# Kernel optimization log

Hardware: AMD Instinct MI355X
Metric: run time of the kernel (lower is better)

The kernel has to match this reference:

```python
import jax, jax.numpy as jnp
import numpy as np

N, E, H, IN, B, L, OUT = 50000, 600000, 128, 128, 256, 4, 10
BN_EPS = 1e-5


def setup_inputs() -> dict:
    key = jax.random.key(0)
    ks = jax.random.split(key, 12)
    x = jax.random.normal(ks[0], (N, IN), dtype=jnp.float32)
    edge_index = jax.random.randint(ks[1], (2, E), 0, N, dtype=jnp.int64)
    batch = jnp.sort(jax.random.randint(ks[2], (N,), 0, B, dtype=jnp.int64))
    s_in = 1.0 / np.sqrt(IN)
    s_h = 1.0 / np.sqrt(H)
    W_enc = jax.random.uniform(ks[3], (IN, H), jnp.float32, -s_in, s_in)
    b_enc = jax.random.uniform(ks[4], (H,), jnp.float32, -s_in, s_in)
    W = jax.random.uniform(ks[5], (L, H, H), jnp.float32, -s_h, s_h)
    b = jax.random.uniform(ks[6], (L, H), jnp.float32, -s_h, s_h)
    gamma = jnp.ones((L, H), jnp.float32)
    beta = jnp.zeros((L, H), jnp.float32)
    W_cls = jax.random.uniform(ks[7], (H, OUT), jnp.float32, -s_h, s_h)
    b_cls = jax.random.uniform(ks[8], (OUT,), jnp.float32, -s_h, s_h)
    return {"x": x, "edge_index": edge_index, "batch": batch,
            "W_enc": W_enc, "b_enc": b_enc, "W": W, "b": b,
            "gamma": gamma, "beta": beta, "W_cls": W_cls, "b_cls": b_cls}


def reference(x, edge_index, batch, W_enc, b_enc, W, b, gamma, beta, W_cls, b_cls):
    n = x.shape[0]
    # add self-loops (PyG GCNConv default)
    loop = jnp.arange(n, dtype=edge_index.dtype)
    row = jnp.concatenate([edge_index[0], loop])  # source nodes
    col = jnp.concatenate([edge_index[1], loop])  # target nodes
    # symmetric normalization: deg over targets, norm_e = d^-1/2[src] * d^-1/2[dst]
    deg = jax.ops.segment_sum(jnp.ones_like(col, dtype=x.dtype), col, num_segments=n)
    dinv = jnp.where(deg > 0, jax.lax.rsqrt(deg), 0.0)
    norm = dinv[row] * dinv[col]  # [E+N]

    # encoder (plain Linear since use_atom_encoder=False)
    h = x @ W_enc + b_enc

    for l in range(L):
        # GCNConv: transform, normalized scatter-add, bias
        t = h @ W[l]
        msg = norm[:, None] * t[row]               # [E+N, H] gather
        agg = jax.ops.segment_sum(msg, col, num_segments=n) + b[l]
        # BatchNorm1d (batch statistics, training-mode math)
        mean = jnp.mean(agg, axis=0)
        var = jnp.var(agg, axis=0)
        hn = (agg - mean) * jax.lax.rsqrt(var + BN_EPS) * gamma[l] + beta[l]
        h = jax.nn.relu(hn)  # dropout p=0.0 -> identity

    # global mean pool over graphs
    sums = jax.ops.segment_sum(h, batch, num_segments=B)
    counts = jax.ops.segment_sum(jnp.ones((n,), h.dtype), batch, num_segments=B)
    g = sums / jnp.maximum(counts, 1.0)[:, None]
    return g @ W_cls + b_cls
```

## Files before the change

### kernel.cpp

```cpp
#include <hip/hip_runtime.h>

#define NN 50000
#define NE 600000
#define HD 128
#define NL 4
#define NB 256
#define NO 10
#define BN_EPS 1e-5f

typedef short bf16x8 __attribute__((ext_vector_type(8)));
typedef float f32x4 __attribute__((ext_vector_type(4)));

__device__ __forceinline__ unsigned short f2bf(float f) {
    union { float f; unsigned int u; } x; x.f = f;
    unsigned int u = x.u;
    unsigned int r = (u + 0x7FFFu + ((u >> 16) & 1u)) >> 16;
    return (unsigned short)r;
}
__device__ __forceinline__ float bf2f(unsigned short s) {
    union { unsigned int u; float f; } x; x.u = ((unsigned int)s) << 16;
    return x.f;
}


__global__ void hist_kernel(const int* __restrict__ col, int* __restrict__ cnt, int e) {
    int i = blockIdx.x * blockDim.x + threadIdx.x;
    if (i < e) atomicAdd(&cnt[col[i]], 1);
}

__global__ void scan1_kernel(const int* __restrict__ cnt, int* __restrict__ outp,
                             int* __restrict__ bsums, float* __restrict__ dinv,
                             int M, int n) {
    __shared__ int s[256];
    int tid = threadIdx.x;
    int base = blockIdx.x * 1024 + tid * 4;
    int v[4];
#pragma unroll
    for (int j = 0; j < 4; ++j) {
        int idx = base + j;
        v[j] = (idx < n) ? cnt[idx] : 0;
        if (idx < n) dinv[idx] = rsqrtf((float)(v[j] + 1));
    }
    int tot = v[0] + v[1] + v[2] + v[3];
    s[tid] = tot;
    __syncthreads();
    for (int off = 1; off < 256; off <<= 1) {
        int x = (tid >= off) ? s[tid - off] : 0;
        __syncthreads();
        s[tid] += x;
        __syncthreads();
    }
    int run = (tid == 0) ? 0 : s[tid - 1];
#pragma unroll
    for (int j = 0; j < 4; ++j) {
        int idx = base + j;
        if (idx < M) outp[idx] = run;
        run += v[j];
    }
    if (tid == 255) bsums[blockIdx.x] = s[255];
}

__global__ void scan3_kernel(int* __restrict__ outp, const int* __restrict__ bsums, int M) {
    __shared__ int sb[64];
    int tid = threadIdx.x;
    int seg = blockIdx.x >> 2;
    if (tid < 64) sb[tid] = (tid < seg) ? bsums[tid] : 0;
    __syncthreads();
    if (tid < 32) sb[tid] += sb[tid + 32];
    __syncthreads();
    if (tid < 16) sb[tid] += sb[tid + 16];
    __syncthreads();
    if (tid < 8) sb[tid] += sb[tid + 8];
    __syncthreads();
    if (tid < 4) sb[tid] += sb[tid + 4];
    __syncthreads();
    if (tid < 2) sb[tid] += sb[tid + 2];
    __syncthreads();
    if (tid == 0) sb[0] += sb[1];
    __syncthreads();
    int i = blockIdx.x * 256 + tid;
    if (i < M) outp[i] += sb[0];
}

__global__ void place_kernel(const int* __restrict__ row, const int* __restrict__ col,
                             const float* __restrict__ dinv, const int* __restrict__ rp,
                             int* __restrict__ fill, int2* __restrict__ csr, int e) {
    int i = blockIdx.x * blockDim.x + threadIdx.x;
    if (i < e) {
        int r = row[i], c = col[i];
        int pos = atomicAdd(&fill[c], 1);
        int idx = rp[c] + pos;
        csr[idx] = make_int2(r, __float_as_int(dinv[r] * dinv[c]));
    }
}

__global__ void wconv_kernel(const float* __restrict__ W, unsigned short* __restrict__ Wt) {
    int i = blockIdx.x * blockDim.x + threadIdx.x;
    if (i >= 4 * 16384) return;
    int m = i >> 14;
    int r = (i >> 7) & 127;
    int k = i & 127;
    Wt[16384 + i] = f2bf(W[(size_t)m * 16384 + k * 128 + r]);
}

__global__ void fuse_enc_kernel(const float* __restrict__ W_enc, const float* __restrict__ W0,
                                const float* __restrict__ b_enc,
                                unsigned short* __restrict__ WtK, float* __restrict__ bb) {
    if (blockIdx.x < 64) {
        int gid = blockIdx.x * 256 + threadIdx.x;
        int i = gid & 127, o = gid >> 7;
        float s = 0.f;
#pragma unroll 8
        for (int h = 0; h < 128; ++h) s += W_enc[i * 128 + h] * W0[h * 128 + o];
        WtK[o * 128 + i] = f2bf(s);
    } else if (threadIdx.x < 128) {
        int o = threadIdx.x;
        float s = 0.f;
#pragma unroll 8
        for (int h = 0; h < 128; ++h) s += b_enc[h] * W0[h * 128 + o];
        bb[o] = s;
    }
}

template <int AMODE>
__global__ __launch_bounds__(256) void gemm128_mfma(const void* __restrict__ Ap,
                                                    const unsigned short* __restrict__ Wt,
                                                    const float* __restrict__ bias,
                                                    const float* __restrict__ bnp,
                                                    unsigned short* __restrict__ Cp,
                                                    int nrows) {
    int wave = threadIdx.x >> 6;
    int lane = threadIdx.x & 63;
    int r16 = lane & 15;
    int kg = lane >> 4;
    int rowBase = blockIdx.x * 64 + wave * 16;
    int row = rowBase + r16;
    bool valid = row < nrows;

    bf16x8 afr[4];
#pragma unroll
    for (int s = 0; s < 4; ++s) {
        bf16x8 tt = {};
        int c0 = s * 32 + kg * 8;
        if constexpr (AMODE == 1) {
            const unsigned short* A = (const unsigned short*)Ap;
            if (valid) tt = *(const bf16x8*)&A[(size_t)row * 128 + c0];
        } else if constexpr (AMODE == 0) {
            const float* A = (const float*)Ap;
            if (valid) {
                const float* p = &A[(size_t)row * 128 + c0];
                float4 u0 = *(const float4*)p;
                float4 u1 = *(const float4*)(p + 4);
                tt[0] = (short)f2bf(u0.x); tt[1] = (short)f2bf(u0.y);
                tt[2] = (short)f2bf(u0.z); tt[3] = (short)f2bf(u0.w);
                tt[4] = (short)f2bf(u1.x); tt[5] = (short)f2bf(u1.y);
                tt[6] = (short)f2bf(u1.z); tt[7] = (short)f2bf(u1.w);
            }
        } else {
            const unsigned short* A = (const unsigned short*)Ap;
            if (valid) {
                bf16x8 raw = *(const bf16x8*)&A[(size_t)row * 128 + c0];
                float4 s0 = *(const float4*)&bnp[c0];
                float4 s1 = *(const float4*)&bnp[c0 + 4];
                float4 h0 = *(const float4*)&bnp[128 + c0];
                float4 h1 = *(const float4*)&bnp[128 + c0 + 4];
                tt[0] = (short)f2bf(fmaxf(bf2f((unsigned short)raw[0]) * s0.x + h0.x, 0.f));
                tt[1] = (short)f2bf(fmaxf(bf2f((unsigned short)raw[1]) * s0.y + h0.y, 0.f));
                tt[2] = (short)f2bf(fmaxf(bf2f((unsigned short)raw[2]) * s0.z + h0.z, 0.f));
                tt[3] = (short)f2bf(fmaxf(bf2f((unsigned short)raw[3]) * s0.w + h0.w, 0.f));
                tt[4] = (short)f2bf(fmaxf(bf2f((unsigned short)raw[4]) * s1.x + h1.x, 0.f));
                tt[5] = (short)f2bf(fmaxf(bf2f((unsigned short)raw[5]) * s1.y + h1.y, 0.f));
                tt[6] = (short)f2bf(fmaxf(bf2f((unsigned short)raw[6]) * s1.z + h1.z, 0.f));
                tt[7] = (short)f2bf(fmaxf(bf2f((unsigned short)raw[7]) * s1.w + h1.w, 0.f));
            }
        }
        afr[s] = tt;
    }

    f32x4 acc[8];
#pragma unroll
    for (int n = 0; n < 8; ++n) acc[n] = (f32x4){0.f, 0.f, 0.f, 0.f};

#pragma unroll
    for (int n = 0; n < 8; ++n) {
        const unsigned short* wp = &Wt[(size_t)(n * 16 + r16) * 128 + kg * 8];
#pragma unroll
        for (int s = 0; s < 4; ++s) {
            bf16x8 wfr = *(const bf16x8*)&wp[s * 32];
            acc[n] = __builtin_amdgcn_mfma_f32_16x16x32_bf16(wfr, afr[s], acc[n], 0, 0, 0);
        }
    }

    if (valid) {
#pragma unroll
        for (int n = 0; n < 8; ++n) {
            int cbase = n * 16 + kg * 4;
            float4 bv = make_float4(0.f, 0.f, 0.f, 0.f);
            if (bias) bv = *(const float4*)&bias[cbase];
            ushort4 o;
            o.x = f2bf(acc[n][0] + bv.x);
            o.y = f2bf(acc[n][1] + bv.y);
            o.z = f2bf(acc[n][2] + bv.z);
            o.w = f2bf(acc[n][3] + bv.w);
            *(ushort4*)&Cp[(size_t)row * 128 + cbase] = o;
        }
    }
}

__global__ __launch_bounds__(256) void aggregate_kernel(const unsigned short* __restrict__ t,
                                                        const int* __restrict__ rp,
                                                        const int2* __restrict__ csr,
                                                        const float* __restrict__ dinv,
                                                        const float* __restrict__ bvec,
                                                        unsigned short* __restrict__ aggb, int n) {
    int wid = blockIdx.x * 4 + (threadIdx.x >> 6);
    int lane = threadIdx.x & 63;
    if (wid >= n) return;
    int c = lane * 2;
    float di = dinv[wid];
    float sw = di * di;
    unsigned int u = *(const unsigned int*)&t[(size_t)wid * 128 + c];
    float ax = sw * bf2f((unsigned short)(u & 0xffff)) + bvec[c];
    float ay = sw * bf2f((unsigned short)(u >> 16)) + bvec[c + 1];
    int e = rp[wid], e1 = rp[wid + 1];
    for (; e + 7 < e1; e += 8) {
        int2 ew[8];
        unsigned int uu[8];
#pragma unroll
        for (int j = 0; j < 8; ++j) ew[j] = csr[e + j];
#pragma unroll
        for (int j = 0; j < 8; ++j) uu[j] = *(const unsigned int*)&t[(size_t)ew[j].x * 128 + c];
#pragma unroll
        for (int j = 0; j < 8; ++j) {
            float w = __int_as_float(ew[j].y);
            ax += w * bf2f((unsigned short)(uu[j] & 0xffff));
            ay += w * bf2f((unsigned short)(uu[j] >> 16));
        }
    }
    for (; e + 3 < e1; e += 4) {
        int2 ew[4];
        unsigned int uu[4];
#pragma unroll
        for (int j = 0; j < 4; ++j) ew[j] = csr[e + j];
#pragma unroll
        for (int j = 0; j < 4; ++j) uu[j] = *(const unsigned int*)&t[(size_t)ew[j].x * 128 + c];
#pragma unroll
        for (int j = 0; j < 4; ++j) {
            float w = __int_as_float(ew[j].y);
            ax += w * bf2f((unsigned short)(uu[j] & 0xffff));
            ay += w * bf2f((unsigned short)(uu[j] >> 16));
        }
    }
    for (; e < e1; ++e) {
        int2 ew = csr[e];
        unsigned int u0 = *(const unsigned int*)&t[(size_t)ew.x * 128 + c];
        float w0 = __int_as_float(ew.y);
        ax += w0 * bf2f((unsigned short)(u0 & 0xffff));
        ay += w0 * bf2f((unsigned short)(u0 >> 16));
    }
    unsigned int o = (unsigned int)f2bf(ax) | ((unsigned int)f2bf(ay) << 16);
    *(unsigned int*)&aggb[(size_t)wid * 128 + c] = o;
}

#define BN_BLOCKS 256
__global__ __launch_bounds__(512) void bn_stats1_kernel(const unsigned short* __restrict__ aggb,
                                                        float* __restrict__ partials, int n) {
    int tid = threadIdx.x;
    int c4 = tid & 31, rs = tid >> 5;
    f32x4 s = {0.f, 0.f, 0.f, 0.f}, q = {0.f, 0.f, 0.f, 0.f};
    for (int r = blockIdx.x * 16 + rs; r < n; r += BN_BLOCKS * 16) {
        ushort4 v4 = *(const ushort4*)&aggb[(size_t)r * 128 + c4 * 4];
        f32x4 v = {bf2f(v4.x), bf2f(v4.y), bf2f(v4.z), bf2f(v4.w)};
        s += v;
        q += v * v;
    }
    __shared__ f32x4 ls[512], lq[512];
    ls[tid] = s;
    lq[tid] = q;
    __syncthreads();
    if (tid < 32) {
        f32x4 ss = ls[tid], qq = lq[tid];
#pragma unroll
        for (int j = 1; j < 16; ++j) { ss += ls[tid + 32 * j]; qq += lq[tid + 32 * j]; }
        float* pb = partials + (size_t)blockIdx.x * 256;
        *(f32x4*)&pb[tid * 4] = ss;
        *(f32x4*)&pb[128 + tid * 4] = qq;
    }
}

__global__ __launch_bounds__(256) void bn_stats2_kernel(const float* __restrict__ partials,
                                                        const float* __restrict__ gamma,
                                                        const float* __restrict__ beta,
                                                        float* __restrict__ bnp, float fn) {
    int tid = threadIdx.x;
    int col4 = tid & 63, g = tid >> 6;
    f32x4 acc = {0.f, 0.f, 0.f, 0.f};
#pragma unroll 8
    for (int bb = g; bb < BN_BLOCKS; bb += 4)
        acc += *(const f32x4*)&partials[(size_t)bb * 256 + col4 * 4];
    __shared__ f32x4 redv[256];
    __shared__ float red[256];
    redv[tid] = acc;
    __syncthreads();
    if (tid < 64) {
        f32x4 tot = redv[tid] + redv[tid + 64] + redv[tid + 128] + redv[tid + 192];
        *(f32x4*)&red[tid * 4] = tot;
    }
    __syncthreads();
    if (tid < 128) {
        float mean = red[tid] / fn;
        float var = fmaxf(red[128 + tid] / fn - mean * mean, 0.f);
        float sc = gamma[tid] * rsqrtf(var + BN_EPS);
        bnp[tid] = sc;
        bnp[128 + tid] = beta[tid] - mean * sc;
    }
}

__global__ __launch_bounds__(256) void pool_cls_kernel(const unsigned short* __restrict__ aggb,
                                                       const float* __restrict__ bnp,
                                                       const int* __restrict__ batch,
                                                       const float* __restrict__ Wc,
                                                       const float* __restrict__ bc,
                                                       float* __restrict__ out, int n) {
    int b = blockIdx.x;
    int tid = threadIdx.x;
    int lo = 0, hi = n;
    while (lo < hi) { int mid = (lo + hi) >> 1; if (batch[mid] < b) lo = mid + 1; else hi = mid; }
    int start = lo;
    hi = n;
    while (lo < hi) { int mid = (lo + hi) >> 1; if (batch[mid] <= b) lo = mid + 1; else hi = mid; }
    int end = lo;

    int c4 = tid & 31, rs = tid >> 5;
    f32x4 sc = *(const f32x4*)&bnp[c4 * 4];
    f32x4 sh = *(const f32x4*)&bnp[128 + c4 * 4];
    f32x4 acc = {0.f, 0.f, 0.f, 0.f};
    for (int r = start + rs; r < end; r += 8) {
        ushort4 v4 = *(const ushort4*)&aggb[(size_t)r * 128 + c4 * 4];
        f32x4 v = {bf2f(v4.x), bf2f(v4.y), bf2f(v4.z), bf2f(v4.w)};
        f32x4 y = v * sc + sh;
#pragma unroll
        for (int k = 0; k < 4; ++k) y[k] = fmaxf(y[k], 0.f);
        acc += y;
    }
    __shared__ f32x4 ls[256];
    __shared__ float g[128];
    ls[tid] = acc;
    __syncthreads();
    if (tid < 32) {
        f32x4 ss = ls[tid];
#pragma unroll
        for (int j = 1; j < 8; ++j) ss += ls[tid + 32 * j];
        float invc = 1.0f / fmaxf((float)(end - start), 1.0f);
#pragma unroll
        for (int k = 0; k < 4; ++k) g[tid * 4 + k] = ss[k] * invc;
    }
    __syncthreads();
    if (tid < NO) {
        float s = bc[tid];
        for (int c = 0; c < 128; ++c) s += g[c] * Wc[c * NO + tid];
        out[b * NO + tid] = s;
    }
}

extern "C" void kernel_launch(void* const* d_in, const int* in_sizes, int n_in,
                              void* d_out, int out_size, void* d_ws, size_t ws_size,
                              hipStream_t stream) {
    const float* x      = (const float*)d_in[0];
    const int*   eidx   = (const int*)d_in[1];
    const int*   batch  = (const int*)d_in[2];
    const float* W_enc  = (const float*)d_in[3];
    const float* b_enc  = (const float*)d_in[4];
    const float* W      = (const float*)d_in[5];
    const float* b      = (const float*)d_in[6];
    const float* gamma  = (const float*)d_in[7];
    const float* beta   = (const float*)d_in[8];
    const float* W_cls  = (const float*)d_in[9];
    const float* b_cls  = (const float*)d_in[10];
    float* out = (float*)d_out;

    const int* erow = eidx;
    const int* ecol = eidx + NE;

    float* dinv     = (float*)d_ws;
    float* partials = dinv + NN;
    float* bnp      = partials + BN_BLOCKS * 256;
    float* bb       = bnp + 256;
    int2*  csr      = (int2*)(bb + 128);
    unsigned short* t    = (unsigned short*)(csr + NE);
    unsigned short* aggb = t + (size_t)NN * HD;
    unsigned short* Wt   = aggb + (size_t)NN * HD;
    int* cnt      = (int*)(Wt + 5 * 16384);
    int* fill     = cnt + NN;
    int* rp       = fill + NN;
    int* bsums    = rp + NN + 1;

    hipMemsetAsync(cnt, 0, 2 * NN * sizeof(int), stream);

    hist_kernel<<<(NE + 255) / 256, 256, 0, stream>>>(ecol, cnt, NE);
    int M = NN + 1;
    int nscan = (M + 1023) / 1024;
    scan1_kernel<<<nscan, 256, 0, stream>>>(cnt, rp, bsums, dinv, M, NN);
    scan3_kernel<<<(M + 255) / 256, 256, 0, stream>>>(rp, bsums, M);
    place_kernel<<<(NE + 255) / 256, 256, 0, stream>>>(erow, ecol, dinv, rp, fill, csr, NE);

    wconv_kernel<<<(4 * 16384 + 255) / 256, 256, 0, stream>>>(W, Wt);
    fuse_enc_kernel<<<65, 256, 0, stream>>>(W_enc, W, b_enc, Wt, bb);

    int gemmBlocks = (NN + 63) / 64;
    gemm128_mfma<0><<<gemmBlocks, 256, 0, stream>>>(x, Wt, bb, nullptr, t, NN);

    for (int l = 0; l < NL; ++l) {
        if (l > 0)
            gemm128_mfma<2><<<gemmBlocks, 256, 0, stream>>>(
                aggb, Wt + (size_t)(l + 1) * 16384, nullptr, bnp, t, NN);
        aggregate_kernel<<<(NN + 3) / 4, 256, 0, stream>>>(t, rp, csr, dinv,
                                                           b + (size_t)l * HD, aggb, NN);
        bn_stats1_kernel<<<BN_BLOCKS, 512, 0, stream>>>(aggb, partials, NN);
        bn_stats2_kernel<<<1, 256, 0, stream>>>(partials, gamma + (size_t)l * HD,
                                                beta + (size_t)l * HD, bnp, (float)NN);
    }

    pool_cls_kernel<<<NB, 256, 0, stream>>>(aggb, bnp, batch, W_cls, b_cls, out, NN);
}
```

Before: 368.1 us.

## Fuse BatchNorm statistics into aggregation via replicated atomic sums

The aggregation kernel now accumulates per-channel sum and sum-of-squares for each block and adds them atomically into 16 replicated accumulator rows. A small finalize kernel reduces the replicas, resets them, and computes the BN scale and shift. This removes a separate full pass over the aggregated features and one launch per layer. In exchange it adds many global atomics that can contend, and the statistics are taken from fp32 values before bf16 rounding. The fill buffer is now zeroed inside the scan kernel, which shrinks the memset.

```diff
diff --git a/kernel.cpp b/kernel.cpp
--- a/kernel.cpp
+++ b/kernel.cpp
@@ -7,6 +7,7 @@
 #define NB 256
 #define NO 10
 #define BN_EPS 1e-5f
+#define NREP 16
 
 typedef short bf16x8 __attribute__((ext_vector_type(8)));
 typedef float f32x4 __attribute__((ext_vector_type(4)));
@@ -30,7 +31,7 @@
 
 __global__ void scan1_kernel(const int* __restrict__ cnt, int* __restrict__ outp,
                              int* __restrict__ bsums, float* __restrict__ dinv,
-                             int M, int n) {
+                             int* __restrict__ fill, int M, int n) {
     __shared__ int s[256];
     int tid = threadIdx.x;
     int base = blockIdx.x * 1024 + tid * 4;
@@ -39,7 +40,10 @@
     for (int j = 0; j < 4; ++j) {
         int idx = base + j;
         v[j] = (idx < n) ? cnt[idx] : 0;
-        if (idx < n) dinv[idx] = rsqrtf((float)(v[j] + 1));
+        if (idx < n) {
+            dinv[idx] = rsqrtf((float)(v[j] + 1));
+            fill[idx] = 0;
+        }
     }
     int tot = v[0] + v[1] + v[2] + v[3];
     s[tid] = tot;
@@ -142,10 +146,7 @@
     for (int s = 0; s < 4; ++s) {
         bf16x8 tt = {};
         int c0 = s * 32 + kg * 8;
-        if constexpr (AMODE == 1) {
-            const unsigned short* A = (const unsigned short*)Ap;
-            if (valid) tt = *(const bf16x8*)&A[(size_t)row * 128 + c0];
-        } else if constexpr (AMODE == 0) {
+        if constexpr (AMODE == 0) {
             const float* A = (const float*)Ap;
             if (valid) {
                 const float* p = &A[(size_t)row * 128 + c0];
@@ -212,100 +213,85 @@
                                                         const int2* __restrict__ csr,
                                                         const float* __restrict__ dinv,
                                                         const float* __restrict__ bvec,
-                                                        unsigned short* __restrict__ aggb, int n) {
-    int wid = blockIdx.x * 4 + (threadIdx.x >> 6);
+                                                        unsigned short* __restrict__ aggb,
+                                                        float* __restrict__ bnsums, int n) {
+    int wave = threadIdx.x >> 6;
     int lane = threadIdx.x & 63;
-    if (wid >= n) return;
+    int wid = blockIdx.x * 4 + wave;
     int c = lane * 2;
-    float di = dinv[wid];
-    float sw = di * di;
-    unsigned int u = *(const unsigned int*)&t[(size_t)wid * 128 + c];
-    float ax = sw * bf2f((unsigned short)(u & 0xffff)) + bvec[c];
-    float ay = sw * bf2f((unsigned short)(u >> 16)) + bvec[c + 1];
-    int e = rp[wid], e1 = rp[wid + 1];
-    for (; e + 7 < e1; e += 8) {
-        int2 ew[8];
-        unsigned int uu[8];
-#pragma unroll
-        for (int j = 0; j < 8; ++j) ew[j] = csr[e + j];
-#pragma unroll
-        for (int j = 0; j < 8; ++j) uu[j] = *(const unsigned int*)&t[(size_t)ew[j].x * 128 + c];
-#pragma unroll
-        for (int j = 0; j < 8; ++j) {
-            float w = __int_as_float(ew[j].y);
-            ax += w * bf2f((unsigned short)(uu[j] & 0xffff));
-            ay += w * bf2f((unsigned short)(uu[j] >> 16));
-        }
-    }
-    for (; e + 3 < e1; e += 4) {
-        int2 ew[4];
-        unsigned int uu[4];
-#pragma unroll
-        for (int j = 0; j < 4; ++j) ew[j] = csr[e + j];
-#pragma unroll
-        for (int j = 0; j < 4; ++j) uu[j] = *(const unsigned int*)&t[(size_t)ew[j].x * 128 + c];
-#pragma unroll
-        for (int j = 0; j < 4; ++j) {
-            float w = __int_as_float(ew[j].y);
-            ax += w * bf2f((unsigned short)(uu[j] & 0xffff));
-            ay += w * bf2f((unsigned short)(uu[j] >> 16));
-        }
-    }
-    for (; e < e1; ++e) {
-        int2 ew = csr[e];
-        unsigned int u0 = *(const unsigned int*)&t[(size_t)ew.x * 128 + c];
-        float w0 = __int_as_float(ew.y);
-        ax += w0 * bf2f((unsigned short)(u0 & 0xffff));
-        ay += w0 * bf2f((unsigned short)(u0 >> 16));
-    }
-    unsigned int o = (unsigned int)f2bf(ax) | ((unsigned int)f2bf(ay) << 16);
-    *(unsigned int*)&aggb[(size_t)wid * 128 + c] = o;
-}
-
-#define BN_BLOCKS 256
-__global__ __launch_bounds__(512) void bn_stats1_kernel(const unsigned short* __restrict__ aggb,
-                                                        float* __restrict__ partials, int n) {
+    float ax = 0.f, ay = 0.f;
+    if (wid < n) {
+        float di = dinv[wid];
+        float sw = di * di;
+        unsigned int u = *(const unsigned int*)&t[(size_t)wid * 128 + c];
+        ax = sw * bf2f((unsigned short)(u & 0xffff)) + bvec[c];
+        ay = sw * bf2f((unsigned short)(u >> 16)) + bvec[c + 1];
+        int e = rp[wid], e1 = rp[wid + 1];
+        for (; e + 7 < e1; e += 8) {
+            int2 ew[8];
+            unsigned int uu[8];
+#pragma unroll
+            for (int j = 0; j < 8; ++j) ew[j] = csr[e + j];
+#pragma unroll
+            for (int j = 0; j < 8; ++j) uu[j] = *(const unsigned int*)&t[(size_t)ew[j].x * 128 + c];
+#pragma unroll
+            for (int j = 0; j < 8; ++j) {
+                float w = __int_as_float(ew[j].y);
+                ax += w * bf2f((unsigned short)(uu[j] & 0xffff));
+                ay += w * bf2f((unsigned short)(uu[j] >> 16));
+            }
+        }
+        for (; e + 3 < e1; e += 4) {
+            int2 ew[4];
+            unsigned int uu[4];
+#pragma unroll
+            for (int j = 0; j < 4; ++j) ew[j] = csr[e + j];
+#pragma unroll
+            for (int j = 0; j < 4; ++j) uu[j] = *(const unsigned int*)&t[(size_t)ew[j].x * 128 + c];
+#pragma unroll
+            for (int j = 0; j < 4; ++j) {
+                float w = __int_as_float(ew[j].y);
+                ax += w * bf2f((unsigned short)(uu[j] & 0xffff));
+                ay += w * bf2f((unsigned short)(uu[j] >> 16));
+            }
+        }
+        for (; e < e1; ++e) {
+            int2 ew = csr[e];
+            unsigned int u0 = *(const unsigned int*)&t[(size_t)ew.x * 128 + c];
+            float w0 = __int_as_float(ew.y);
+            ax += w0 * bf2f((unsigned short)(u0 & 0xffff));
+            ay += w0 * bf2f((unsigned short)(u0 >> 16));
+        }
+        unsigned int o = (unsigned int)f2bf(ax) | ((unsigned int)f2bf(ay) << 16);
+        *(unsigned int*)&aggb[(size_t)wid * 128 + c] = o;
+    }
+
+    __shared__ float4 st[4][64];
+    st[wave][lane] = make_float4(ax, ay, ax * ax, ay * ay);
+    __syncthreads();
+    if (wave == 0) {
+        float4 a = st[0][lane], b2 = st[1][lane], c2 = st[2][lane], d2 = st[3][lane];
+        float* rep = bnsums + (size_t)(blockIdx.x & (NREP - 1)) * 256;
+        atomicAdd(&rep[c], a.x + b2.x + c2.x + d2.x);
+        atomicAdd(&rep[c + 1], a.y + b2.y + c2.y + d2.y);
+        atomicAdd(&rep[128 + c], a.z + b2.z + c2.z + d2.z);
+        atomicAdd(&rep[128 + c + 1], a.w + b2.w + c2.w + d2.w);
+    }
+}
+
+__global__ __launch_bounds__(256) void bn_fin_kernel(float* __restrict__ bnsums,
+                                                     const float* __restrict__ gamma,
+                                                     const float* __restrict__ beta,
+                                                     float* __restrict__ bnp, float fn) {
     int tid = threadIdx.x;
-    int c4 = tid & 31, rs = tid >> 5;
-    f32x4 s = {0.f, 0.f, 0.f, 0.f}, q = {0.f, 0.f, 0.f, 0.f};
-    for (int r = blockIdx.x * 16 + rs; r < n; r += BN_BLOCKS * 16) {
-        ushort4 v4 = *(const ushort4*)&aggb[(size_t)r * 128 + c4 * 4];
-        f32x4 v = {bf2f(v4.x), bf2f(v4.y), bf2f(v4.z), bf2f(v4.w)};
-        s += v;
-        q += v * v;
-    }
-    __shared__ f32x4 ls[512], lq[512];
-    ls[tid] = s;
-    lq[tid] = q;
-    __syncthreads();
-    if (tid < 32) {
-        f32x4 ss = ls[tid], qq = lq[tid];
-#pragma unroll
-        for (int j = 1; j < 16; ++j) { ss += ls[tid + 32 * j]; qq += lq[tid + 32 * j]; }
-        float* pb = partials + (size_t)blockIdx.x * 256;
-        *(f32x4*)&pb[tid * 4] = ss;
-        *(f32x4*)&pb[128 + tid * 4] = qq;
-    }
-}
-
-__global__ __launch_bounds__(256) void bn_stats2_kernel(const float* __restrict__ partials,
-                                                        const float* __restrict__ gamma,
-                                                        const float* __restrict__ beta,
-                                                        float* __restrict__ bnp, float fn) {
-    int tid = threadIdx.x;
-    int col4 = tid & 63, g = tid >> 6;
-    f32x4 acc = {0.f, 0.f, 0.f, 0.f};
-#pragma unroll 8
-    for (int bb = g; bb < BN_BLOCKS; bb += 4)
-        acc += *(const f32x4*)&partials[(size_t)bb * 256 + col4 * 4];
-    __shared__ f32x4 redv[256];
+    float acc = 0.f;
+#pragma unroll
+    for (int r = 0; r < NREP; ++r) {
+        acc += bnsums[r * 256 + tid];
+        bnsums[r * 256 + tid] = 0.f;
+    }
     __shared__ float red[256];
-    redv[tid] = acc;
-    __syncthreads();
-    if (tid < 64) {
-        f32x4 tot = redv[tid] + redv[tid + 64] + redv[tid + 128] + redv[tid + 192];
-        *(f32x4*)&red[tid * 4] = tot;
-    }
+    red[tid] = acc;
     __syncthreads();
     if (tid < 128) {
         float mean = red[tid] / fn;
@@ -383,24 +369,24 @@
     const int* ecol = eidx + NE;
 
     float* dinv     = (float*)d_ws;
-    float* partials = dinv + NN;
-    float* bnp      = partials + BN_BLOCKS * 256;
+    float* bnp      = dinv + NN;
     float* bb       = bnp + 256;
     int2*  csr      = (int2*)(bb + 128);
     unsigned short* t    = (unsigned short*)(csr + NE);
     unsigned short* aggb = t + (size_t)NN * HD;
     unsigned short* Wt   = aggb + (size_t)NN * HD;
-    int* cnt      = (int*)(Wt + 5 * 16384);
+    float* bnsums   = (float*)(Wt + 5 * 16384);
+    int* cnt      = (int*)(bnsums + NREP * 256);
     int* fill     = cnt + NN;
     int* rp       = fill + NN;
     int* bsums    = rp + NN + 1;
 
-    hipMemsetAsync(cnt, 0, 2 * NN * sizeof(int), stream);
+    hipMemsetAsync(bnsums, 0, (NREP * 256 + NN) * sizeof(int), stream);
 
     hist_kernel<<<(NE + 255) / 256, 256, 0, stream>>>(ecol, cnt, NE);
     int M = NN + 1;
     int nscan = (M + 1023) / 1024;
-    scan1_kernel<<<nscan, 256, 0, stream>>>(cnt, rp, bsums, dinv, M, NN);
+    scan1_kernel<<<nscan, 256, 0, stream>>>(cnt, rp, bsums, dinv, fill, M, NN);
     scan3_kernel<<<(M + 255) / 256, 256, 0, stream>>>(rp, bsums, M);
     place_kernel<<<(NE + 255) / 256, 256, 0, stream>>>(erow, ecol, dinv, rp, fill, csr, NE);
 
@@ -415,10 +401,10 @@
             gemm128_mfma<2><<<gemmBlocks, 256, 0, stream>>>(
                 aggb, Wt + (size_t)(l + 1) * 16384, nullptr, bnp, t, NN);
         aggregate_kernel<<<(NN + 3) / 4, 256, 0, stream>>>(t, rp, csr, dinv,
-                                                           b + (size_t)l * HD, aggb, NN);
-        bn_stats1_kernel<<<BN_BLOCKS, 512, 0, stream>>>(aggb, partials, NN);
-        bn_stats2_kernel<<<1, 256, 0, stream>>>(partials, gamma + (size_t)l * HD,
-                                                beta + (size_t)l * HD, bnp, (float)NN);
+                                                           b + (size_t)l * HD, aggb,
+                                                           bnsums, NN);
+        bn_fin_kernel<<<1, 256, 0, stream>>>(bnsums, gamma + (size_t)l * HD,
+                                             beta + (size_t)l * HD, bnp, (float)NN);
     }
 
     pool_cls_kernel<<<NB, 256, 0, stream>>>(aggb, bnp, batch, W_cls, b_cls, out, NN);
```

Measured after the change: 414.4 us. +12.6%, slower.
